# Performance work log

Hardware: AMD Instinct MI355X
Metric: run time of the kernel (lower is better)

## Reference

```python
import jax, jax.numpy as jnp
import numpy as np

B, S, H = 1, 2048, 2048
I = 1408            # moe intermediate size
E = 16              # n_routed_experts
K = 6               # num_experts_per_tok
G = 4               # n_group
KG = 2              # topk_group
NSH = 2             # n_shared_experts -> shared intermediate = NSH*I
RSF = 2.5           # routed_scaling_factor
CAP = 2 * (B * S * K) // E


def setup_inputs() -> dict:
    key = jax.random.key(0)
    ks = jax.random.split(key, 9)
    sh = NSH * I
    s_h = 1.0 / np.sqrt(H).astype(np.float32)
    s_i = 1.0 / np.sqrt(I).astype(np.float32)
    s_s = 1.0 / np.sqrt(sh).astype(np.float32)
    return {
        "x": jax.random.normal(ks[0], (B, S, H), jnp.float32),
        "gate_w": jax.random.normal(ks[1], (E, H), jnp.float32) * s_h,
        "gate_bias": jnp.zeros((E,), jnp.float32),
        "w_gate": jax.random.normal(ks[2], (E, H, I), jnp.float32) * s_h,
        "w_up": jax.random.normal(ks[3], (E, H, I), jnp.float32) * s_h,
        "w_down": jax.random.normal(ks[4], (E, I, H), jnp.float32) * s_i,
        "ws_gate": jax.random.normal(ks[5], (H, sh), jnp.float32) * s_h,
        "ws_up": jax.random.normal(ks[6], (H, sh), jnp.float32) * s_h,
        "ws_down": jax.random.normal(ks[7], (sh, H), jnp.float32) * s_s,
    }


def _gate(x2d, gate_w, gate_bias):
    # MoEGate: fp32 linear -> sigmoid -> noaux_tc group-limited top-k
    logits = x2d.astype(jnp.float32) @ gate_w.astype(jnp.float32).T     # [T,E]
    scores = jax.nn.sigmoid(logits)
    scores_c = scores + gate_bias                                       # e_score_correction_bias
    T = scores.shape[0]
    gs = scores_c.reshape(T, G, E // G)
    top2, _ = jax.lax.top_k(gs, 2)
    group_scores = top2.sum(-1)                                         # [T,G] sum of top-2 per group
    _, gidx = jax.lax.top_k(group_scores, KG)                           # keep top KG groups
    gmask = jnp.zeros((T, G), scores.dtype).at[jnp.arange(T)[:, None], gidx].set(1.0)
    smask = jnp.repeat(gmask, E // G, axis=1)                           # [T,E]
    tmp = jnp.where(smask > 0, scores_c, 0.0)
    _, topk_idx = jax.lax.top_k(tmp, K)                                 # [T,K]
    topk_w = jnp.take_along_axis(scores, topk_idx, axis=1)              # weights from UNbiased scores
    topk_w = topk_w / (topk_w.sum(-1, keepdims=True) + 1e-20)           # norm_topk_prob
    topk_w = topk_w * RSF
    return topk_idx, topk_w


def reference(x, gate_w, gate_bias, w_gate, w_up, w_down, ws_gate, ws_up, ws_down):
    T = B * S
    x2d = x.reshape(T, H)
    topk_idx, topk_w = _gate(x2d, gate_w, gate_bias)

    # ---- dispatch: sort (token,k) assignments by expert id (grouped-GEMM layout) ----
    flat_e = topk_idx.reshape(-1)                       # [T*K]
    order = jnp.argsort(flat_e, stable=True)
    sorted_e = flat_e[order]
    counts = jnp.bincount(flat_e, length=E)             # batch_sizes per expert
    starts = jnp.concatenate([jnp.zeros((1,), counts.dtype), jnp.cumsum(counts)[:-1]])
    pos = jnp.arange(T * K) - starts[sorted_e]          # slot within expert bucket
    tok = order // K                                    # source token of each assignment
    buf = jnp.zeros((E, CAP, H), x.dtype).at[sorted_e, pos].set(x2d[tok], mode="drop")

    # ---- grouped SwiGLU expert FFN (gmm equivalent) ----
    g = jnp.einsum("ech,ehi->eci", buf, w_gate)
    u = jnp.einsum("ech,ehi->eci", buf, w_up)
    y_e = jnp.einsum("eci,eih->ech", jax.nn.silu(g) * u, w_down)

    # ---- combine: gather back, weight, scatter-add per token ----
    keep = (pos < CAP).astype(x.dtype)
    y_sorted = y_e[sorted_e, jnp.minimum(pos, CAP - 1)] * keep[:, None]
    w_flat = topk_w.reshape(-1)[order]
    y = jnp.zeros((T, H), x.dtype).at[tok].add(y_sorted * w_flat[:, None])

    # ---- shared experts (dense SwiGLU on all tokens) ----
    sg = x2d @ ws_gate
    su = x2d @ ws_up
    y = y + (jax.nn.silu(sg) * su) @ ws_down
    return y.reshape(B, S, H)
```

## Files before the change

kernel.cpp:

```cpp
#include <hip/hip_runtime.h>

typedef unsigned short u16;
typedef u16  u16x8 __attribute__((ext_vector_type(8)));
typedef u16  u16x4 __attribute__((ext_vector_type(4)));
typedef short s16x8 __attribute__((ext_vector_type(8)));
typedef float f32x4 __attribute__((ext_vector_type(4)));

static constexpr int TT   = 2048;
static constexpr int HD   = 2048;
static constexpr int ID   = 1408;
static constexpr int NE   = 16;
static constexpr int TOPK = 6;
static constexpr int CAPE = 1536;
static constexpr int SHD  = 2816;
static constexpr float RSF_ = 2.5f;

__device__ __forceinline__ u16 f2b(float f) {
  unsigned int u = __builtin_bit_cast(unsigned int, f);
  unsigned int r = (u + 0x7FFFu + ((u >> 16) & 1u)) >> 16;
  return (u16)r;
}
__device__ __forceinline__ float b2f(u16 u) {
  unsigned int v = ((unsigned int)u) << 16;
  return __builtin_bit_cast(float, v);
}

__device__ __forceinline__ void gl_lds16(const u16* gp, u16* lp) {
  __builtin_amdgcn_global_load_lds(
      (const __attribute__((address_space(1))) void*)(unsigned long long)(const void*)gp,
      (__attribute__((address_space(3))) void*)(unsigned int)(unsigned long long)(void*)lp,
      16, 0, 0);
}

__global__ __launch_bounds__(256) void k_cvt(const float* __restrict__ in, u16* __restrict__ out) {
  size_t i = (size_t)blockIdx.x * 256 + threadIdx.x;
  const float4* p = (const float4*)in;
  float4 v0 = p[i * 2], v1 = p[i * 2 + 1];
  u16x8 o = { f2b(v0.x), f2b(v0.y), f2b(v0.z), f2b(v0.w),
              f2b(v1.x), f2b(v1.y), f2b(v1.z), f2b(v1.w) };
  *(u16x8*)(out + i * 8) = o;
}

__global__ __launch_bounds__(256) void k_gate2(const float* __restrict__ x,
    const float* __restrict__ gw, const float* __restrict__ gb,
    int* __restrict__ topk_idx, float* __restrict__ topk_w) {
  const int t = threadIdx.x;
  const int tok0 = blockIdx.x * 8;
  const int i  = t >> 5;
  const int sub = t & 31;
  const int e  = sub & 15;
  const int kh = sub >> 4;
  const float4* xr = (const float4*)(x + (size_t)(tok0 + i) * HD) + kh * (HD / 8);
  const float4* wr = (const float4*)(gw + (size_t)e * HD) + kh * (HD / 8);
  float acc = 0.f;
  #pragma unroll 8
  for (int k = 0; k < HD / 8; ++k) {
    float4 a = xr[k], b = wr[k];
    acc += a.x * b.x + a.y * b.y;
    acc += a.z * b.z + a.w * b.w;
  }
  acc += __shfl_down(acc, 16);
  __shared__ float lg[8][16];
  if (sub < 16) lg[i][e] = acc;
  __syncthreads();
  if (t >= 8) return;
  const int tok = tok0 + t;
  float s[NE], sc[NE];
  #pragma unroll
  for (int ee = 0; ee < NE; ++ee) {
    s[ee]  = 1.f / (1.f + expf(-lg[t][ee]));
    sc[ee] = s[ee] + gb[ee];
  }
  float gs[4];
  #pragma unroll
  for (int g = 0; g < 4; ++g) {
    float m1 = -1e30f, m2 = -1e30f;
    #pragma unroll
    for (int j = 0; j < 4; ++j) {
      float v = sc[g * 4 + j];
      if (v > m1) { m2 = m1; m1 = v; } else if (v > m2) m2 = v;
    }
    gs[g] = m1 + m2;
  }
  int g0 = 0;
  #pragma unroll
  for (int g = 1; g < 4; ++g) if (gs[g] > gs[g0]) g0 = g;
  int g1 = -1; float g1v = -1e30f;
  #pragma unroll
  for (int g = 0; g < 4; ++g) {
    if (g == g0) continue;
    if (g1 < 0 || gs[g] > g1v) { g1 = g; g1v = gs[g]; }
  }
  float tmp[NE];
  #pragma unroll
  for (int ee = 0; ee < NE; ++ee) {
    int g = ee >> 2;
    tmp[ee] = (g == g0 || g == g1) ? sc[ee] : 0.0f;
  }
  unsigned used = 0;
  float wsum = 0.f;
  int idxs[TOPK]; float wv[TOPK];
  #pragma unroll
  for (int k = 0; k < TOPK; ++k) {
    int best = -1; float bv = -2e30f;
    #pragma unroll
    for (int ee = 0; ee < NE; ++ee) {
      bool ok = (((used >> ee) & 1u) == 0u) && (tmp[ee] > bv);
      if (ok) { bv = tmp[ee]; best = ee; }
    }
    used |= 1u << best;
    float sv = 0.f;
    #pragma unroll
    for (int ee = 0; ee < NE; ++ee) if (ee == best) sv = s[ee];
    idxs[k] = best; wv[k] = sv; wsum += sv;
  }
  float scale = RSF_ / (wsum + 1e-20f);
  #pragma unroll
  for (int k = 0; k < TOPK; ++k) {
    topk_idx[tok * TOPK + k] = idxs[k];
    topk_w[tok * TOPK + k]   = wv[k] * scale;
  }
}

__global__ __launch_bounds__(256) void k_count_pos(const int* __restrict__ topk_idx,
    int* __restrict__ rowidx, int* __restrict__ tok_of_row, int* __restrict__ counts) {
  const int e = blockIdx.x, t = threadIdx.x;
  __shared__ int pref[256];
  const int t0 = t * 8;
  int c = 0;
  for (int tt = t0; tt < t0 + 8; ++tt)
    for (int k = 0; k < TOPK; ++k) c += (topk_idx[tt * TOPK + k] == e) ? 1 : 0;
  pref[t] = c;
  __syncthreads();
  for (int off = 1; off < 256; off <<= 1) {
    int v = (t >= off) ? pref[t - off] : 0;
    __syncthreads();
    pref[t] += v;
    __syncthreads();
  }
  int run = pref[t] - c;
  if (t == 255) counts[e] = (pref[255] < CAPE) ? pref[255] : CAPE;
  for (int tt = t0; tt < t0 + 8; ++tt)
    for (int k = 0; k < TOPK; ++k)
      if (topk_idx[tt * TOPK + k] == e) {
        if (run < CAPE) {
          rowidx[tt * TOPK + k] = e * CAPE + run;
          tok_of_row[e * CAPE + run] = tt;
        } else {
          rowidx[tt * TOPK + k] = -1;
        }
        ++run;
      }
}

__global__ __launch_bounds__(256) void k_transpose_cvt(const float* __restrict__ in,
    u16* __restrict__ out, int R, int Cc, long zin, long zout) {
  __shared__ float tile[64][65];
  const float* src = in + (size_t)blockIdx.z * zin;
  u16* dst = out + (size_t)blockIdx.z * zout;
  const int r0 = blockIdx.x * 64, c0 = blockIdx.y * 64, t = threadIdx.x;
  #pragma unroll
  for (int i = 0; i < 4; ++i) {
    int c = t + 256 * i;
    int r = c >> 4, cg = (c & 15) << 2;
    float4 v = *(const float4*)(src + (size_t)(r0 + r) * Cc + c0 + cg);
    tile[r][cg + 0] = v.x; tile[r][cg + 1] = v.y;
    tile[r][cg + 2] = v.z; tile[r][cg + 3] = v.w;
  }
  __syncthreads();
  #pragma unroll
  for (int i = 0; i < 4; ++i) {
    int c = t + 256 * i;
    int oc = c >> 4, og = (c & 15) << 2;
    u16x4 w;
    #pragma unroll
    for (int j = 0; j < 4; ++j) w[j] = f2b(tile[og + j][oc]);
    *(u16x4*)(dst + (size_t)(c0 + oc) * R + r0 + og) = w;
  }
}

template <int EPI>
__global__ __launch_bounds__(256) void k_gemm2(
    const u16* __restrict__ A, const u16* __restrict__ Bt, void* __restrict__ Cptr,
    const u16* __restrict__ aux, const int* __restrict__ row_map,
    const int* __restrict__ counts, int Mfixed, int K, int lda, int ldc,
    long b_stride, int row_cap) {
  unsigned gx = gridDim.x, gy = gridDim.y, gz = gridDim.z;
  unsigned F = (blockIdx.z * gy + blockIdx.y) * gx + blockIdx.x;
  unsigned Nn = gx * gy * gz;
  unsigned q = Nn >> 3, r = Nn & 7;
  unsigned xcd = F & 7, pos = F >> 3;
  unsigned wi = (xcd < r) ? xcd * (q + 1) + pos
                          : r * (q + 1) + (xcd - r) * q + pos;
  unsigned bx = wi % gx, tq = wi / gx;
  unsigned by = tq % gy, bz = tq / gy;

  const int e = bz;
  const int cnt = counts ? counts[e] : Mfixed;
  const int M_e = counts ? (cnt < row_cap ? cnt : row_cap) : Mfixed;
  const int m0 = bx * 128;
  if (m0 >= M_e) return;
  const int n0 = by * 128;
  const int row_base = counts ? e * row_cap : 0;
  const u16* Bte = Bt + (size_t)e * b_stride;

  __shared__ __align__(16) u16 As[2][128 * 32];
  __shared__ __align__(16) u16 Bs[2][128 * 32];

  const int t = threadIdx.x;
  const int l = t & 63, w = t >> 6;
  const int wm = (w >> 1) * 64, wn = (w & 1) * 64;

  const u16 *ap[2], *bp[2];
  int loff[2];
  #pragma unroll
  for (int i = 0; i < 2; ++i) {
    int c = t + 256 * i;
    int row = c >> 2, g = c & 3;
    int kg = g ^ ((row >> 1) & 3);
    loff[i] = c * 8;
    int rg = m0 + row; if (rg > M_e - 1) rg = M_e - 1;
    int arow = row_map ? row_map[row_base + rg] : row_base + rg;
    ap[i] = A + (size_t)arow * lda + kg * 8;
    bp[i] = Bte + (size_t)(n0 + row) * K + kg * 8;
  }

  f32x4 acc[4][4];
  #pragma unroll
  for (int m = 0; m < 4; ++m)
    #pragma unroll
    for (int n = 0; n < 4; ++n) acc[m][n] = f32x4{0, 0, 0, 0};

  const int l15 = l & 15, g0 = l >> 4;
  int aoff[4], boff[4];
  #pragma unroll
  for (int i = 0; i < 4; ++i) {
    int rA = wm + i * 16 + l15;
    int rB = wn + i * 16 + l15;
    aoff[i] = rA * 64 + ((g0 ^ ((rA >> 1) & 3)) << 4);
    boff[i] = rB * 64 + ((g0 ^ ((rB >> 1) & 3)) << 4);
  }

  const int nk = K >> 5;
  #pragma unroll
  for (int i = 0; i < 2; ++i) {
    gl_lds16(ap[i], &As[0][loff[i]]); ap[i] += 32;
    gl_lds16(bp[i], &Bs[0][loff[i]]); bp[i] += 32;
  }
  __syncthreads();
  int cur = 0;
  for (int ks = 0; ks < nk; ++ks) {
    if (ks + 1 < nk) {
      #pragma unroll
      for (int i = 0; i < 2; ++i) {
        gl_lds16(ap[i], &As[cur ^ 1][loff[i]]); ap[i] += 32;
        gl_lds16(bp[i], &Bs[cur ^ 1][loff[i]]); bp[i] += 32;
      }
    }
    s16x8 af[4], bfr[4];
    #pragma unroll
    for (int i = 0; i < 4; ++i) {
      af[i]  = __builtin_bit_cast(s16x8, *(const u16x8*)((const char*)As[cur] + aoff[i]));
      bfr[i] = __builtin_bit_cast(s16x8, *(const u16x8*)((const char*)Bs[cur] + boff[i]));
    }
    #pragma unroll
    for (int m = 0; m < 4; ++m)
      #pragma unroll
      for (int n = 0; n < 4; ++n)
        acc[m][n] = __builtin_amdgcn_mfma_f32_16x16x32_bf16(af[m], bfr[n], acc[m][n], 0, 0, 0);
    __syncthreads();
    cur ^= 1;
  }

  const int cl = l15, rw = g0 * 4;
  #pragma unroll
  for (int m = 0; m < 4; ++m) {
    #pragma unroll
    for (int n = 0; n < 4; ++n) {
      f32x4 v = acc[m][n];
      int gr0 = m0 + wm + m * 16 + rw;
      int gc  = n0 + wn + n * 16 + cl;
      #pragma unroll
      for (int j = 0; j < 4; ++j) {
        int rr = gr0 + j;
        if (rr < M_e) {
          size_t ci = (size_t)(row_base + rr) * ldc + gc;
          if (EPI == 1) {
            ((float*)Cptr)[ci] = v[j];
          } else if (EPI == 2) {
            float gf = b2f(aux[ci]);
            float act = gf / (1.f + __expf(-gf)) * v[j];
            ((u16*)Cptr)[ci] = f2b(act);
          } else {
            ((u16*)Cptr)[ci] = f2b(v[j]);
          }
        }
      }
    }
  }
}

__global__ __launch_bounds__(256) void k_combine(const u16* __restrict__ down,
    const int* __restrict__ rowidx, const float* __restrict__ tw,
    float* __restrict__ out) {
  const int t = blockIdx.x, l = threadIdx.x;
  __shared__ int rid[TOPK];
  __shared__ float wk[TOPK];
  if (l < TOPK) { rid[l] = rowidx[t * TOPK + l]; wk[l] = tw[t * TOPK + l]; }
  __syncthreads();
  const int h0 = l * 8;
  float* op = out + (size_t)t * HD + h0;
  float4 o0 = *(float4*)op, o1 = *(float4*)(op + 4);
  float a[8] = { o0.x, o0.y, o0.z, o0.w, o1.x, o1.y, o1.z, o1.w };
  #pragma unroll
  for (int k = 0; k < TOPK; ++k) {
    int r = rid[k];
    if (r < 0) continue;
    float wkk = wk[k];
    u16x8 v = *(const u16x8*)(down + (size_t)r * HD + h0);
    #pragma unroll
    for (int j = 0; j < 8; ++j) a[j] += wkk * b2f(v[j]);
  }
  o0 = make_float4(a[0], a[1], a[2], a[3]);
  o1 = make_float4(a[4], a[5], a[6], a[7]);
  *(float4*)op = o0;
  *(float4*)(op + 4) = o1;
}

__global__ __launch_bounds__(256) void k_sentinel(float* o, int n) {
  int i = blockIdx.x * 256 + threadIdx.x;
  if (i < n) o[i] = 12345.0f;
}

extern "C" void kernel_launch(void* const* d_in, const int* in_sizes, int n_in,
                              void* d_out, int out_size, void* d_ws, size_t ws_size,
                              hipStream_t stream) {
  const float* x       = (const float*)d_in[0];
  const float* gate_w  = (const float*)d_in[1];
  const float* gate_b  = (const float*)d_in[2];
  const float* w_gate  = (const float*)d_in[3];
  const float* w_up    = (const float*)d_in[4];
  const float* w_down  = (const float*)d_in[5];
  const float* ws_gate = (const float*)d_in[6];
  const float* ws_up   = (const float*)d_in[7];
  const float* ws_down = (const float*)d_in[8];
  float* out = (float*)d_out;

  char* base = (char*)d_ws;
  char* p = base;
  auto alloc = [&](size_t bytes) -> char* {
    char* r = p;
    p += (bytes + 255) & ~(size_t)255;
    return r;
  };
  u16* wT    = (u16*)alloc((size_t)NE * ID * HD * 2);
  u16* swT   = (u16*)alloc((size_t)SHD * HD * 2);
  u16* xb    = (u16*)alloc((size_t)TT * HD * 2);
  u16* gbuf  = (u16*)alloc((size_t)NE * CAPE * ID * 2);
  u16* dbuf  = (u16*)alloc((size_t)NE * CAPE * HD * 2);
  u16* sgb   = (u16*)alloc((size_t)TT * SHD * 2);
  int*   tidx  = (int*)alloc((size_t)TT * TOPK * 4);
  float* twv   = (float*)alloc((size_t)TT * TOPK * 4);
  int*   ridx  = (int*)alloc((size_t)TT * TOPK * 4);
  int*   torow = (int*)alloc((size_t)NE * CAPE * 4);
  int*   cnts  = (int*)alloc(64);

  if ((size_t)(p - base) > ws_size) {
    k_sentinel<<<dim3((out_size + 255) / 256), dim3(256), 0, stream>>>(out, out_size);
    return;
  }

  dim3 b256(256);

  k_cvt<<<dim3((TT * HD) / (8 * 256)), b256, 0, stream>>>(x, xb);
  k_gate2<<<dim3(TT / 8), b256, 0, stream>>>(x, gate_w, gate_b, tidx, twv);
  k_count_pos<<<dim3(NE), b256, 0, stream>>>(tidx, ridx, torow, cnts);

  k_transpose_cvt<<<dim3(HD / 64, ID / 64, NE), b256, 0, stream>>>(
      w_gate, wT, HD, ID, (long)HD * ID, (long)ID * HD);
  k_gemm2<0><<<dim3(CAPE / 128, ID / 128, NE), b256, 0, stream>>>(
      xb, wT, gbuf, nullptr, torow, cnts, 0, HD, HD, ID, (long)ID * HD, CAPE);
  k_transpose_cvt<<<dim3(HD / 64, ID / 64, NE), b256, 0, stream>>>(
      w_up, wT, HD, ID, (long)HD * ID, (long)ID * HD);
  k_gemm2<2><<<dim3(CAPE / 128, ID / 128, NE), b256, 0, stream>>>(
      xb, wT, gbuf, gbuf, torow, cnts, 0, HD, HD, ID, (long)ID * HD, CAPE);
  k_transpose_cvt<<<dim3(ID / 64, HD / 64, NE), b256, 0, stream>>>(
      w_down, wT, ID, HD, (long)ID * HD, (long)HD * ID);
  k_gemm2<0><<<dim3(CAPE / 128, HD / 128, NE), b256, 0, stream>>>(
      gbuf, wT, dbuf, nullptr, nullptr, cnts, 0, ID, ID, HD, (long)HD * ID, CAPE);

  k_transpose_cvt<<<dim3(HD / 64, SHD / 64, 1), b256, 0, stream>>>(ws_gate, swT, HD, SHD, 0, 0);
  k_gemm2<0><<<dim3(TT / 128, SHD / 128, 1), b256, 0, stream>>>(
      xb, swT, sgb, nullptr, nullptr, nullptr, TT, HD, HD, SHD, 0, 0);
  k_transpose_cvt<<<dim3(HD / 64, SHD / 64, 1), b256, 0, stream>>>(ws_up, swT, HD, SHD, 0, 0);
  k_gemm2<2><<<dim3(TT / 128, SHD / 128, 1), b256, 0, stream>>>(
      xb, swT, sgb, sgb, nullptr, nullptr, TT, HD, HD, SHD, 0, 0);
  k_transpose_cvt<<<dim3(SHD / 64, HD / 64, 1), b256, 0, stream>>>(ws_down, swT, SHD, HD, 0, 0);
  k_gemm2<1><<<dim3(TT / 128, HD / 128, 1), b256, 0, stream>>>(
      sgb, swT, out, nullptr, nullptr, nullptr, TT, SHD, SHD, HD, 0, 0);

  k_combine<<<dim3(TT), b256, 0, stream>>>(dbuf, ridx, twv, out);
}
```

Baseline: 751.4 us.

## Triple-buffer GEMM LDS tiles with explicit vmcnt waits and raw barriers

The bf16 MFMA GEMM moves from double to triple buffering of its A/B shared-memory tiles, prefetching two k-steps ahead. Explicit s_waitcnt vmcnt values and raw s_barrier with sched_barrier replace __syncthreads, so only the oldest tile's loads are waited on. This aims to hide global-to-LDS load latency behind the MFMA work. It raises LDS use from 32KB to 48KB per block, which may cut occupancy, and the hand-set vmcnt counts assume exactly four loads per stage.

```diff
diff --git a/kernel.cpp b/kernel.cpp
--- a/kernel.cpp
+++ b/kernel.cpp
@@ -180,7 +180,7 @@
 }
 
 template <int EPI>
-__global__ __launch_bounds__(256) void k_gemm2(
+__global__ __launch_bounds__(256) void k_gemm4(
     const u16* __restrict__ A, const u16* __restrict__ Bt, void* __restrict__ Cptr,
     const u16* __restrict__ aux, const int* __restrict__ row_map,
     const int* __restrict__ counts, int Mfixed, int K, int lda, int ldc,
@@ -204,8 +204,8 @@
   const int row_base = counts ? e * row_cap : 0;
   const u16* Bte = Bt + (size_t)e * b_stride;
 
-  __shared__ __align__(16) u16 As[2][128 * 32];
-  __shared__ __align__(16) u16 Bs[2][128 * 32];
+  __shared__ __align__(16) u16 As[3][128 * 32];
+  __shared__ __align__(16) u16 Bs[3][128 * 32];
 
   const int t = threadIdx.x;
   const int l = t & 63, w = t >> 6;
@@ -247,29 +247,49 @@
     gl_lds16(ap[i], &As[0][loff[i]]); ap[i] += 32;
     gl_lds16(bp[i], &Bs[0][loff[i]]); bp[i] += 32;
   }
-  __syncthreads();
-  int cur = 0;
+  #pragma unroll
+  for (int i = 0; i < 2; ++i) {
+    gl_lds16(ap[i], &As[1][loff[i]]); ap[i] += 32;
+    gl_lds16(bp[i], &Bs[1][loff[i]]); bp[i] += 32;
+  }
+
+  int bcur = 0, bst = 2;
   for (int ks = 0; ks < nk; ++ks) {
-    if (ks + 1 < nk) {
+    if (ks + 2 < nk) {
+      u16* Ad = &As[0][0] + bst * (128 * 32);
+      u16* Bd = &Bs[0][0] + bst * (128 * 32);
       #pragma unroll
       for (int i = 0; i < 2; ++i) {
-        gl_lds16(ap[i], &As[cur ^ 1][loff[i]]); ap[i] += 32;
-        gl_lds16(bp[i], &Bs[cur ^ 1][loff[i]]); bp[i] += 32;
+        gl_lds16(ap[i], Ad + loff[i]); ap[i] += 32;
+        gl_lds16(bp[i], Bd + loff[i]); bp[i] += 32;
       }
+      asm volatile("s_waitcnt vmcnt(8)" ::: "memory");
+    } else if (ks + 1 < nk) {
+      asm volatile("s_waitcnt vmcnt(4)" ::: "memory");
+    } else {
+      asm volatile("s_waitcnt vmcnt(0)" ::: "memory");
     }
+    __builtin_amdgcn_s_barrier();
+    __builtin_amdgcn_sched_barrier(0);
+
+    const char* Ab = (const char*)(&As[0][0] + bcur * (128 * 32));
+    const char* Bb = (const char*)(&Bs[0][0] + bcur * (128 * 32));
     s16x8 af[4], bfr[4];
     #pragma unroll
     for (int i = 0; i < 4; ++i) {
-      af[i]  = __builtin_bit_cast(s16x8, *(const u16x8*)((const char*)As[cur] + aoff[i]));
-      bfr[i] = __builtin_bit_cast(s16x8, *(const u16x8*)((const char*)Bs[cur] + boff[i]));
+      af[i]  = __builtin_bit_cast(s16x8, *(const u16x8*)(Ab + aoff[i]));
+      bfr[i] = __builtin_bit_cast(s16x8, *(const u16x8*)(Bb + boff[i]));
     }
     #pragma unroll
     for (int m = 0; m < 4; ++m)
       #pragma unroll
       for (int n = 0; n < 4; ++n)
         acc[m][n] = __builtin_amdgcn_mfma_f32_16x16x32_bf16(af[m], bfr[n], acc[m][n], 0, 0, 0);
-    __syncthreads();
-    cur ^= 1;
+
+    __builtin_amdgcn_sched_barrier(0);
+    __builtin_amdgcn_s_barrier();
+    bcur = (bcur == 2) ? 0 : bcur + 1;
+    bst  = (bst  == 2) ? 0 : bst  + 1;
   }
 
   const int cl = l15, rw = g0 * 4;
@@ -378,25 +398,25 @@
 
   k_transpose_cvt<<<dim3(HD / 64, ID / 64, NE), b256, 0, stream>>>(
       w_gate, wT, HD, ID, (long)HD * ID, (long)ID * HD);
-  k_gemm2<0><<<dim3(CAPE / 128, ID / 128, NE), b256, 0, stream>>>(
+  k_gemm4<0><<<dim3(CAPE / 128, ID / 128, NE), b256, 0, stream>>>(
       xb, wT, gbuf, nullptr, torow, cnts, 0, HD, HD, ID, (long)ID * HD, CAPE);
   k_transpose_cvt<<<dim3(HD / 64, ID / 64, NE), b256, 0, stream>>>(
       w_up, wT, HD, ID, (long)HD * ID, (long)ID * HD);
-  k_gemm2<2><<<dim3(CAPE / 128, ID / 128, NE), b256, 0, stream>>>(
+  k_gemm4<2><<<dim3(CAPE / 128, ID / 128, NE), b256, 0, stream>>>(
       xb, wT, gbuf, gbuf, torow, cnts, 0, HD, HD, ID, (long)ID * HD, CAPE);
   k_transpose_cvt<<<dim3(ID / 64, HD / 64, NE), b256, 0, stream>>>(
       w_down, wT, ID, HD, (long)ID * HD, (long)HD * ID);
-  k_gemm2<0><<<dim3(CAPE / 128, HD / 128, NE), b256, 0, stream>>>(
+  k_gemm4<0><<<dim3(CAPE / 128, HD / 128, NE), b256, 0, stream>>>(
       gbuf, wT, dbuf, nullptr, nullptr, cnts, 0, ID, ID, HD, (long)HD * ID, CAPE);
 
   k_transpose_cvt<<<dim3(HD / 64, SHD / 64, 1), b256, 0, stream>>>(ws_gate, swT, HD, SHD, 0, 0);
-  k_gemm2<0><<<dim3(TT / 128, SHD / 128, 1), b256, 0, stream>>>(
+  k_gemm4<0><<<dim3(TT / 128, SHD / 128, 1), b256, 0, stream>>>(
       xb, swT, sgb, nullptr, nullptr, nullptr, TT, HD, HD, SHD, 0, 0);
   k_transpose_cvt<<<dim3(HD / 64, SHD / 64, 1), b256, 0, stream>>>(ws_up, swT, HD, SHD, 0, 0);
-  k_gemm2<2><<<dim3(TT / 128, SHD / 128, 1), b256, 0, stream>>>(
+  k_gemm4<2><<<dim3(TT / 128, SHD / 128, 1), b256, 0, stream>>>(
       xb, swT, sgb, sgb, nullptr, nullptr, TT, HD, HD, SHD, 0, 0);
   k_transpose_cvt<<<dim3(SHD / 64, HD / 64, 1), b256, 0, stream>>>(ws_down, swT, SHD, HD, 0, 0);
-  k_gemm2<1><<<dim3(TT / 128, HD / 128, 1), b256, 0, stream>>>(
+  k_gemm4<1><<<dim3(TT / 128, HD / 128, 1), b256, 0, stream>>>(
       sgb, swT, out, nullptr, nullptr, nullptr, TT, SHD, SHD, HD, 0, 0);
 
   k_combine<<<dim3(TT), b256, 0, stream>>>(dbuf, ridx, twv, out);
```

Result: no change. 737.3 us (-1.9%).

## Fuse fp32 weight conversion into GEMM loads with persistent atomic tile scheduler

Applied to the files above, without the earlier changes.

Removes the separate transpose-and-convert kernels for all six weight matrices. The GEMM now reads fp32 weights directly, converts them to bf16 in registers and stores them transposed into padded LDS rows. The launch also becomes a persistent 768-block grid that takes tiles from an atomic counter, so tiles belonging to empty expert rows are skipped cheaply. The trade-off is that the weight tile is re-read and re-converted once per M-tile instead of once per call. The B operand also goes through registers instead of direct-to-LDS loads, which adds VGPR pressure and LDS write work inside the loop.

```diff
diff --git a/kernel.cpp b/kernel.cpp
--- a/kernel.cpp
+++ b/kernel.cpp
@@ -2,7 +2,6 @@
 
 typedef unsigned short u16;
 typedef u16  u16x8 __attribute__((ext_vector_type(8)));
-typedef u16  u16x4 __attribute__((ext_vector_type(4)));
 typedef short s16x8 __attribute__((ext_vector_type(8)));
 typedef float f32x4 __attribute__((ext_vector_type(4)));
 
@@ -14,6 +13,8 @@
 static constexpr int CAPE = 1536;
 static constexpr int SHD  = 2816;
 static constexpr float RSF_ = 2.5f;
+static constexpr int PGRID = 768;
+static constexpr int BROW = 72;
 
 __device__ __forceinline__ u16 f2b(float f) {
   unsigned int u = __builtin_bit_cast(unsigned int, f);
@@ -30,6 +31,18 @@
       (const __attribute__((address_space(1))) void*)(unsigned long long)(const void*)gp,
       (__attribute__((address_space(3))) void*)(unsigned int)(unsigned long long)(void*)lp,
       16, 0, 0);
+}
+
+__device__ __forceinline__ void swz_map(int idx, int ntot, int mtiles, int ntiles,
+                                        int& bx, int& by, int& e) {
+  unsigned q = (unsigned)ntot >> 3, r = (unsigned)ntot & 7;
+  unsigned xcd = (unsigned)idx & 7, pos = (unsigned)idx >> 3;
+  unsigned wi = (xcd < r) ? xcd * (q + 1) + pos
+                          : r * (q + 1) + (xcd - r) * q + pos;
+  bx = wi % mtiles;
+  unsigned tq = wi / mtiles;
+  by = tq % ntiles;
+  e  = tq / ntiles;
 }
 
 __global__ __launch_bounds__(256) void k_cvt(const float* __restrict__ in, u16* __restrict__ out) {
@@ -39,6 +52,10 @@
   u16x8 o = { f2b(v0.x), f2b(v0.y), f2b(v0.z), f2b(v0.w),
               f2b(v1.x), f2b(v1.y), f2b(v1.z), f2b(v1.w) };
   *(u16x8*)(out + i * 8) = o;
+}
+
+__global__ __launch_bounds__(64) void k_init(int* c) {
+  if (threadIdx.x < 16) c[threadIdx.x] = 0;
 }
 
 __global__ __launch_bounds__(256) void k_gate2(const float* __restrict__ x,
@@ -153,146 +170,156 @@
       }
 }
 
-__global__ __launch_bounds__(256) void k_transpose_cvt(const float* __restrict__ in,
-    u16* __restrict__ out, int R, int Cc, long zin, long zout) {
-  __shared__ float tile[64][65];
-  const float* src = in + (size_t)blockIdx.z * zin;
-  u16* dst = out + (size_t)blockIdx.z * zout;
-  const int r0 = blockIdx.x * 64, c0 = blockIdx.y * 64, t = threadIdx.x;
-  #pragma unroll
-  for (int i = 0; i < 4; ++i) {
-    int c = t + 256 * i;
-    int r = c >> 4, cg = (c & 15) << 2;
-    float4 v = *(const float4*)(src + (size_t)(r0 + r) * Cc + c0 + cg);
-    tile[r][cg + 0] = v.x; tile[r][cg + 1] = v.y;
-    tile[r][cg + 2] = v.z; tile[r][cg + 3] = v.w;
-  }
-  __syncthreads();
-  #pragma unroll
-  for (int i = 0; i < 4; ++i) {
-    int c = t + 256 * i;
-    int oc = c >> 4, og = (c & 15) << 2;
-    u16x4 w;
-    #pragma unroll
-    for (int j = 0; j < 4; ++j) w[j] = f2b(tile[og + j][oc]);
-    *(u16x4*)(dst + (size_t)(c0 + oc) * R + r0 + og) = w;
-  }
-}
-
 template <int EPI>
-__global__ __launch_bounds__(256) void k_gemm2(
-    const u16* __restrict__ A, const u16* __restrict__ Bt, void* __restrict__ Cptr,
+__global__ __launch_bounds__(256) void k_pfuse(
+    const u16* __restrict__ A, const float* __restrict__ W, void* __restrict__ Cptr,
     const u16* __restrict__ aux, const int* __restrict__ row_map,
-    const int* __restrict__ counts, int Mfixed, int K, int lda, int ldc,
-    long b_stride, int row_cap) {
-  unsigned gx = gridDim.x, gy = gridDim.y, gz = gridDim.z;
-  unsigned F = (blockIdx.z * gy + blockIdx.y) * gx + blockIdx.x;
-  unsigned Nn = gx * gy * gz;
-  unsigned q = Nn >> 3, r = Nn & 7;
-  unsigned xcd = F & 7, pos = F >> 3;
-  unsigned wi = (xcd < r) ? xcd * (q + 1) + pos
-                          : r * (q + 1) + (xcd - r) * q + pos;
-  unsigned bx = wi % gx, tq = wi / gx;
-  unsigned by = tq % gy, bz = tq / gy;
-
-  const int e = bz;
-  const int cnt = counts ? counts[e] : Mfixed;
-  const int M_e = counts ? (cnt < row_cap ? cnt : row_cap) : Mfixed;
-  const int m0 = bx * 128;
-  if (m0 >= M_e) return;
-  const int n0 = by * 128;
-  const int row_base = counts ? e * row_cap : 0;
-  const u16* Bte = Bt + (size_t)e * b_stride;
-
-  __shared__ __align__(16) u16 As[2][128 * 32];
-  __shared__ __align__(16) u16 Bs[2][128 * 32];
-
+    const int* __restrict__ counts, int Mfixed, int Ncols, int K, int lda, int ldc,
+    long w_stride, int row_cap, int mtiles, int ntiles, int nexp,
+    int* __restrict__ counter) {
   const int t = threadIdx.x;
   const int l = t & 63, w = t >> 6;
   const int wm = (w >> 1) * 64, wn = (w & 1) * 64;
-
-  const u16 *ap[2], *bp[2];
-  int loff[2];
-  #pragma unroll
-  for (int i = 0; i < 2; ++i) {
-    int c = t + 256 * i;
-    int row = c >> 2, g = c & 3;
-    int kg = g ^ ((row >> 1) & 3);
-    loff[i] = c * 8;
-    int rg = m0 + row; if (rg > M_e - 1) rg = M_e - 1;
-    int arow = row_map ? row_map[row_base + rg] : row_base + rg;
-    ap[i] = A + (size_t)arow * lda + kg * 8;
-    bp[i] = Bte + (size_t)(n0 + row) * K + kg * 8;
-  }
-
-  f32x4 acc[4][4];
-  #pragma unroll
-  for (int m = 0; m < 4; ++m)
-    #pragma unroll
-    for (int n = 0; n < 4; ++n) acc[m][n] = f32x4{0, 0, 0, 0};
-
   const int l15 = l & 15, g0 = l >> 4;
-  int aoff[4], boff[4];
+
+  __shared__ __align__(16) u16 As[2][128 * 32];
+  __shared__ __align__(16) char Bs[2][128 * BROW];
+  __shared__ int s_tile;
+
+  int aoff[4];
   #pragma unroll
   for (int i = 0; i < 4; ++i) {
     int rA = wm + i * 16 + l15;
+    aoff[i] = rA * 64 + ((g0 ^ ((rA >> 1) & 3)) << 4);
+  }
+  int boff[4];
+  #pragma unroll
+  for (int i = 0; i < 4; ++i) {
     int rB = wn + i * 16 + l15;
-    aoff[i] = rA * 64 + ((g0 ^ ((rA >> 1) & 3)) << 4);
-    boff[i] = rB * 64 + ((g0 ^ ((rB >> 1) & 3)) << 4);
-  }
-
+    boff[i] = rB * BROW + g0 * 16;
+  }
+  const int bk0 = (t >> 5) * 4, bn0 = (t & 31) * 4;
+  const int bwoff = bn0 * BROW + bk0 * 2;
+
+  const int ntot = mtiles * ntiles * nexp;
   const int nk = K >> 5;
-  #pragma unroll
-  for (int i = 0; i < 2; ++i) {
-    gl_lds16(ap[i], &As[0][loff[i]]); ap[i] += 32;
-    gl_lds16(bp[i], &Bs[0][loff[i]]); bp[i] += 32;
-  }
-  __syncthreads();
-  int cur = 0;
-  for (int ks = 0; ks < nk; ++ks) {
-    if (ks + 1 < nk) {
-      #pragma unroll
-      for (int i = 0; i < 2; ++i) {
-        gl_lds16(ap[i], &As[cur ^ 1][loff[i]]); ap[i] += 32;
-        gl_lds16(bp[i], &Bs[cur ^ 1][loff[i]]); bp[i] += 32;
-      }
-    }
-    s16x8 af[4], bfr[4];
-    #pragma unroll
-    for (int i = 0; i < 4; ++i) {
-      af[i]  = __builtin_bit_cast(s16x8, *(const u16x8*)((const char*)As[cur] + aoff[i]));
-      bfr[i] = __builtin_bit_cast(s16x8, *(const u16x8*)((const char*)Bs[cur] + boff[i]));
-    }
+  const int cl = l15, rw = g0 * 4;
+
+  for (;;) {
+    if (t == 0) s_tile = atomicAdd(counter, 1);
+    __syncthreads();
+    int idx = s_tile;
+    __syncthreads();
+    if (idx >= ntot) break;
+    int bx, by, e;
+    swz_map(idx, ntot, mtiles, ntiles, bx, by, e);
+    const int cnt = counts ? counts[e] : Mfixed;
+    const int M_e = counts ? (cnt < row_cap ? cnt : row_cap) : Mfixed;
+    const int m0 = bx * 128;
+    if (m0 >= M_e) continue;
+    const int n0b = by * 128;
+    const int row_base = counts ? e * row_cap : 0;
+    const float* We = W + (size_t)e * w_stride;
+    const float* bsrc = We + (size_t)bk0 * Ncols + n0b + bn0;
+
+    const u16 *ap[2];
+    int loffA[2];
+    #pragma unroll
+    for (int i = 0; i < 2; ++i) {
+      int c = t + 256 * i;
+      int row = c >> 2, g = c & 3;
+      int kg = g ^ ((row >> 1) & 3);
+      loffA[i] = c * 8;
+      int rg = m0 + row; if (rg > M_e - 1) rg = M_e - 1;
+      int arow = row_map ? row_map[row_base + rg] : row_base + rg;
+      ap[i] = A + (size_t)arow * lda + kg * 8;
+    }
+
+    f32x4 acc[4][4];
     #pragma unroll
     for (int m = 0; m < 4; ++m)
       #pragma unroll
-      for (int n = 0; n < 4; ++n)
-        acc[m][n] = __builtin_amdgcn_mfma_f32_16x16x32_bf16(af[m], bfr[n], acc[m][n], 0, 0, 0);
+      for (int n = 0; n < 4; ++n) acc[m][n] = f32x4{0, 0, 0, 0};
+
+    #pragma unroll
+    for (int i = 0; i < 2; ++i) { gl_lds16(ap[i], &As[0][loffA[i]]); ap[i] += 32; }
+    {
+      float4 bq0 = *(const float4*)(bsrc);
+      float4 bq1 = *(const float4*)(bsrc + Ncols);
+      float4 bq2 = *(const float4*)(bsrc + 2 * Ncols);
+      float4 bq3 = *(const float4*)(bsrc + 3 * Ncols);
+      char* bb = &Bs[0][bwoff];
+      #pragma unroll
+      for (int i = 0; i < 4; ++i) {
+        float e0 = (&bq0.x)[i], e1 = (&bq1.x)[i], e2 = (&bq2.x)[i], e3 = (&bq3.x)[i];
+        uint2 wv;
+        wv.x = (unsigned)f2b(e0) | ((unsigned)f2b(e1) << 16);
+        wv.y = (unsigned)f2b(e2) | ((unsigned)f2b(e3) << 16);
+        *(uint2*)(bb + i * BROW) = wv;
+      }
+    }
     __syncthreads();
-    cur ^= 1;
-  }
-
-  const int cl = l15, rw = g0 * 4;
-  #pragma unroll
-  for (int m = 0; m < 4; ++m) {
-    #pragma unroll
-    for (int n = 0; n < 4; ++n) {
-      f32x4 v = acc[m][n];
-      int gr0 = m0 + wm + m * 16 + rw;
-      int gc  = n0 + wn + n * 16 + cl;
+
+    int cur = 0;
+    for (int kt = 0; kt < nk; ++kt) {
+      const bool have = (kt + 1 < nk);
+      float4 bq0, bq1, bq2, bq3;
+      if (have) {
+        #pragma unroll
+        for (int i = 0; i < 2; ++i) { gl_lds16(ap[i], &As[cur ^ 1][loffA[i]]); ap[i] += 32; }
+        const float* bs = bsrc + (size_t)(kt + 1) * 32 * Ncols;
+        bq0 = *(const float4*)(bs);
+        bq1 = *(const float4*)(bs + Ncols);
+        bq2 = *(const float4*)(bs + 2 * Ncols);
+        bq3 = *(const float4*)(bs + 3 * Ncols);
+      }
+      s16x8 af[4], bfr[4];
       #pragma unroll
-      for (int j = 0; j < 4; ++j) {
-        int rr = gr0 + j;
-        if (rr < M_e) {
-          size_t ci = (size_t)(row_base + rr) * ldc + gc;
-          if (EPI == 1) {
-            ((float*)Cptr)[ci] = v[j];
-          } else if (EPI == 2) {
-            float gf = b2f(aux[ci]);
-            float act = gf / (1.f + __expf(-gf)) * v[j];
-            ((u16*)Cptr)[ci] = f2b(act);
-          } else {
-            ((u16*)Cptr)[ci] = f2b(v[j]);
+      for (int i = 0; i < 4; ++i) {
+        af[i]  = __builtin_bit_cast(s16x8, *(const u16x8*)((const char*)As[cur] + aoff[i]));
+        bfr[i] = __builtin_bit_cast(s16x8, *(const u16x8*)(&Bs[cur][0] + boff[i]));
+      }
+      #pragma unroll
+      for (int m = 0; m < 4; ++m)
+        #pragma unroll
+        for (int n = 0; n < 4; ++n)
+          acc[m][n] = __builtin_amdgcn_mfma_f32_16x16x32_bf16(af[m], bfr[n], acc[m][n], 0, 0, 0);
+      if (have) {
+        char* bb = &Bs[cur ^ 1][bwoff];
+        #pragma unroll
+        for (int i = 0; i < 4; ++i) {
+          float e0 = (&bq0.x)[i], e1 = (&bq1.x)[i], e2 = (&bq2.x)[i], e3 = (&bq3.x)[i];
+          uint2 wv;
+          wv.x = (unsigned)f2b(e0) | ((unsigned)f2b(e1) << 16);
+          wv.y = (unsigned)f2b(e2) | ((unsigned)f2b(e3) << 16);
+          *(uint2*)(bb + i * BROW) = wv;
+        }
+      }
+      __syncthreads();
+      cur ^= 1;
+    }
+
+    #pragma unroll
+    for (int m = 0; m < 4; ++m) {
+      #pragma unroll
+      for (int n = 0; n < 4; ++n) {
+        f32x4 v = acc[m][n];
+        int gr0 = m0 + wm + m * 16 + rw;
+        int gc  = n0b + wn + n * 16 + cl;
+        #pragma unroll
+        for (int j = 0; j < 4; ++j) {
+          int rr = gr0 + j;
+          if (rr < M_e) {
+            size_t ci = (size_t)(row_base + rr) * ldc + gc;
+            if (EPI == 1) {
+              ((float*)Cptr)[ci] = v[j];
+            } else if (EPI == 2) {
+              float gf = b2f(aux[ci]);
+              float act = gf / (1.f + __expf(-gf)) * v[j];
+              ((u16*)Cptr)[ci] = f2b(act);
+            } else {
+              ((u16*)Cptr)[ci] = f2b(v[j]);
+            }
           }
         }
       }
@@ -353,8 +380,6 @@
     p += (bytes + 255) & ~(size_t)255;
     return r;
   };
-  u16* wT    = (u16*)alloc((size_t)NE * ID * HD * 2);
-  u16* swT   = (u16*)alloc((size_t)SHD * HD * 2);
   u16* xb    = (u16*)alloc((size_t)TT * HD * 2);
   u16* gbuf  = (u16*)alloc((size_t)NE * CAPE * ID * 2);
   u16* dbuf  = (u16*)alloc((size_t)NE * CAPE * HD * 2);
@@ -364,6 +389,7 @@
   int*   ridx  = (int*)alloc((size_t)TT * TOPK * 4);
   int*   torow = (int*)alloc((size_t)NE * CAPE * 4);
   int*   cnts  = (int*)alloc(64);
+  int*   ctrs  = (int*)alloc(64);
 
   if ((size_t)(p - base) > ws_size) {
     k_sentinel<<<dim3((out_size + 255) / 256), dim3(256), 0, stream>>>(out, out_size);
@@ -373,31 +399,29 @@
   dim3 b256(256);
 
   k_cvt<<<dim3((TT * HD) / (8 * 256)), b256, 0, stream>>>(x, xb);
+  k_init<<<dim3(1), dim3(64), 0, stream>>>(ctrs);
   k_gate2<<<dim3(TT / 8), b256, 0, stream>>>(x, gate_w, gate_b, tidx, twv);
   k_count_pos<<<dim3(NE), b256, 0, stream>>>(tidx, ridx, torow, cnts);
 
-  k_transpose_cvt<<<dim3(HD / 64, ID / 64, NE), b256, 0, stream>>>(
-      w_gate, wT, HD, ID, (long)HD * ID, (long)ID * HD);
-  k_gemm2<0><<<dim3(CAPE / 128, ID / 128, NE), b256, 0, stream>>>(
-      xb, wT, gbuf, nullptr, torow, cnts, 0, HD, HD, ID, (long)ID * HD, CAPE);
-  k_transpose_cvt<<<dim3(HD / 64, ID / 64, NE), b256, 0, stream>>>(
-      w_up, wT, HD, ID, (long)HD * ID, (long)ID * HD);
-  k_gemm2<2><<<dim3(CAPE / 128, ID / 128, NE), b256, 0, stream>>>(
-      xb, wT, gbuf, gbuf, torow, cnts, 0, HD, HD, ID, (long)ID * HD, CAPE);
-  k_transpose_cvt<<<dim3(ID / 64, HD / 64, NE), b256, 0, stream>>>(
-      w_down, wT, ID, HD, (long)ID * HD, (long)HD * ID);
-  k_gemm2<0><<<dim3(CAPE / 128, HD / 128, NE), b256, 0, stream>>>(
-      gbuf, wT, dbuf, nullptr, nullptr, cnts, 0, ID, ID, HD, (long)HD * ID, CAPE);
-
-  k_transpose_cvt<<<dim3(HD / 64, SHD / 64, 1), b256, 0, stream>>>(ws_gate, swT, HD, SHD, 0, 0);
-  k_gemm2<0><<<dim3(TT / 128, SHD / 128, 1), b256, 0, stream>>>(
-      xb, swT, sgb, nullptr, nullptr, nullptr, TT, HD, HD, SHD, 0, 0);
-  k_transpose_cvt<<<dim3(HD / 64, SHD / 64, 1), b256, 0, stream>>>(ws_up, swT, HD, SHD, 0, 0);
-  k_gemm2<2><<<dim3(TT / 128, SHD / 128, 1), b256, 0, stream>>>(
-      xb, swT, sgb, sgb, nullptr, nullptr, TT, HD, HD, SHD, 0, 0);
-  k_transpose_cvt<<<dim3(SHD / 64, HD / 64, 1), b256, 0, stream>>>(ws_down, swT, SHD, HD, 0, 0);
-  k_gemm2<1><<<dim3(TT / 128, HD / 128, 1), b256, 0, stream>>>(
-      sgb, swT, out, nullptr, nullptr, nullptr, TT, SHD, SHD, HD, 0, 0);
+  k_pfuse<0><<<dim3(PGRID), b256, 0, stream>>>(
+      xb, w_gate, gbuf, nullptr, torow, cnts, 0, ID, HD, HD, ID,
+      (long)HD * ID, CAPE, CAPE / 128, ID / 128, NE, ctrs + 0);
+  k_pfuse<2><<<dim3(PGRID), b256, 0, stream>>>(
+      xb, w_up, gbuf, gbuf, torow, cnts, 0, ID, HD, HD, ID,
+      (long)HD * ID, CAPE, CAPE / 128, ID / 128, NE, ctrs + 1);
+  k_pfuse<0><<<dim3(PGRID), b256, 0, stream>>>(
+      gbuf, w_down, dbuf, nullptr, nullptr, cnts, 0, HD, ID, ID, HD,
+      (long)ID * HD, CAPE, CAPE / 128, HD / 128, NE, ctrs + 2);
+
+  k_pfuse<0><<<dim3(PGRID), b256, 0, stream>>>(
+      xb, ws_gate, sgb, nullptr, nullptr, nullptr, TT, SHD, HD, HD, SHD,
+      0, 0, TT / 128, SHD / 128, 1, ctrs + 3);
+  k_pfuse<2><<<dim3(PGRID), b256, 0, stream>>>(
+      xb, ws_up, sgb, sgb, nullptr, nullptr, TT, SHD, HD, HD, SHD,
+      0, 0, TT / 128, SHD / 128, 1, ctrs + 4);
+  k_pfuse<1><<<dim3(PGRID), b256, 0, stream>>>(
+      sgb, ws_down, out, nullptr, nullptr, nullptr, TT, HD, SHD, SHD, HD,
+      0, 0, TT / 128, HD / 128, 1, ctrs + 5);
 
   k_combine<<<dim3(TT), b256, 0, stream>>>(dbuf, ridx, twv, out);
 }
```

Result: slower. 1.045 ms (+39.1%).
